# Optimization experiments

Measured on AMD Instinct MI355X. Metric: run time of the kernel, lower is better.

## Reference

```python
import jax, jax.numpy as jnp
import numpy as np

HEADS = 16
D_MODEL = 1024
D_HEAD = D_MODEL // HEADS


def setup_inputs() -> dict:
    key = jax.random.key(0)
    ks = jax.random.split(key, 9)
    s_h = 1.0 / np.sqrt(D_HEAD)
    s_m = 1.0 / np.sqrt(D_MODEL)
    return {
        "x": jax.random.normal(ks[0], (4, 2048, D_MODEL), dtype=jnp.float32),
        "Wq": jax.random.uniform(ks[1], (D_HEAD, D_HEAD), jnp.float32, -s_h, s_h),
        "bq": jax.random.uniform(ks[2], (D_HEAD,), jnp.float32, -s_h, s_h),
        "Wk": jax.random.uniform(ks[3], (D_HEAD, D_HEAD), jnp.float32, -s_h, s_h),
        "bk": jax.random.uniform(ks[4], (D_HEAD,), jnp.float32, -s_h, s_h),
        "Wv": jax.random.uniform(ks[5], (D_HEAD, D_HEAD), jnp.float32, -s_h, s_h),
        "bv": jax.random.uniform(ks[6], (D_HEAD,), jnp.float32, -s_h, s_h),
        "Wp": jax.random.uniform(ks[7], (D_MODEL, D_MODEL), jnp.float32, -s_m, s_m),
        "bp": jax.random.uniform(ks[8], (D_MODEL,), jnp.float32, -s_m, s_m),
    }


def reference(x, Wq, bq, Wk, bk, Wv, bv, Wp, bp):
    B, T, C = x.shape
    xh = x.reshape(B, T, HEADS, D_HEAD)  # [B,T,H,Dh]
    # per-head linear projections (torch Linear: x @ W.T + b)
    q = jnp.einsum('bthd,ed->bhte', xh, Wq) + bq  # [B,H,T,Dh]
    k = jnp.einsum('bthd,ed->bhte', xh, Wk) + bk
    v = jnp.einsum('bthd,ed->bhte', xh, Wv) + bv
    # NOTE: original scales by sqrt(C) = sqrt(d_model), not sqrt(d_head)
    att = jnp.einsum('bhqd,bhkd->bhqk', q, k) / jnp.sqrt(jnp.float32(C))
    att = jax.nn.softmax(att, axis=-1)
    out = jnp.einsum('bhqk,bhkd->bhqd', att, v)  # [B,H,T,Dh]
    out = out.transpose(0, 2, 1, 3).reshape(B, T, C)
    return out @ Wp.T + bp
```

## Files before the change

### kernel.cpp

```cpp
#include <hip/hip_runtime.h>
#include <hip/hip_bf16.h>
#include <cstddef>

#define B_  4
#define T_  2048
#define H_  16
#define DH  64
#define C_  1024
#define BH  64

typedef float  f32x16 __attribute__((ext_vector_type(16)));
typedef __bf16 bf16x8 __attribute__((ext_vector_type(8)));

#define MFMA32(a, b, c) __builtin_amdgcn_mfma_f32_32x32x16_bf16(a, b, c, 0, 0, 0)


__global__ __launch_bounds__(256) void qkv_kernel(
    const float* __restrict__ x,
    const float* __restrict__ Wq, const float* __restrict__ bq,
    const float* __restrict__ Wk, const float* __restrict__ bk,
    const float* __restrict__ Wv, const float* __restrict__ bv,
    __bf16* __restrict__ q, __bf16* __restrict__ k, __bf16* __restrict__ vt)
{
    __shared__ __bf16 Xs[128 * 72];
    __shared__ __bf16 Ws[3][64 * 72];
    __bf16* Vtl = Xs;

    const int tt  = blockIdx.x;
    const int bh  = blockIdx.y;
    const int b   = bh >> 4, h = bh & 15;
    const int t0  = tt * 128;
    const int tid = threadIdx.x;
    const int wave = tid >> 6, lane = tid & 63;
    const int m = lane & 31, hh = lane >> 5;

    #pragma unroll
    for (int i = 0; i < 8; ++i) {
        const int idx = i * 256 + tid;
        const int r = idx >> 4, c = (idx & 15) * 4;
        const float4 x4 = *(const float4*)(x + ((size_t)(b * T_ + t0 + r)) * C_ + h * DH + c);
        const uint lo = ((uint)__builtin_bit_cast(unsigned short, (__bf16)x4.y) << 16)
                      | (uint)__builtin_bit_cast(unsigned short, (__bf16)x4.x);
        const uint hi = ((uint)__builtin_bit_cast(unsigned short, (__bf16)x4.w) << 16)
                      | (uint)__builtin_bit_cast(unsigned short, (__bf16)x4.z);
        *(uint*)&Xs[r * 72 + c]     = lo;
        *(uint*)&Xs[r * 72 + c + 2] = hi;
    }
    #pragma unroll
    for (int i = 0; i < 4; ++i) {
        const int idx = i * 256 + tid;
        const int r = idx >> 4, c = (idx & 15) * 4;
        const float* wsrc[3] = {Wq, Wk, Wv};
        #pragma unroll
        for (int wv_ = 0; wv_ < 3; ++wv_) {
            const float4 w4 = *(const float4*)(wsrc[wv_] + r * 64 + c);
            const uint lo = ((uint)__builtin_bit_cast(unsigned short, (__bf16)w4.y) << 16)
                          | (uint)__builtin_bit_cast(unsigned short, (__bf16)w4.x);
            const uint hi = ((uint)__builtin_bit_cast(unsigned short, (__bf16)w4.w) << 16)
                          | (uint)__builtin_bit_cast(unsigned short, (__bf16)w4.z);
            *(uint*)&Ws[wv_][r * 72 + c]     = lo;
            *(uint*)&Ws[wv_][r * 72 + c + 2] = hi;
        }
    }
    __syncthreads();

    bf16x8 xf[4];
    #pragma unroll
    for (int ks = 0; ks < 4; ++ks)
        xf[ks] = *(const bf16x8*)&Xs[(wave * 32 + m) * 72 + ks * 16 + hh * 8];
    __syncthreads();

    const float s32 = 0.03125f;

    #pragma unroll
    for (int mat = 0; mat < 3; ++mat) {
        f32x16 acc0 = {}, acc1 = {};
        #pragma unroll
        for (int ks = 0; ks < 4; ++ks) {
            const bf16x8 w0 = *(const bf16x8*)&Ws[mat][(m) * 72 + ks * 16 + hh * 8];
            const bf16x8 w1 = *(const bf16x8*)&Ws[mat][(32 + m) * 72 + ks * 16 + hh * 8];
            acc0 = MFMA32(xf[ks], w0, acc0);
            acc1 = MFMA32(xf[ks], w1, acc1);
        }
        const float* bias = (mat == 0) ? bq : (mat == 1) ? bk : bv;
        const float b0 = bias[m], b1 = bias[32 + m];
        #pragma unroll
        for (int r = 0; r < 16; ++r) {
            const int R = (r & 3) + 8 * (r >> 2) + 4 * hh;
            const int tloc = wave * 32 + R;
            const float v0 = acc0[r] + b0, v1 = acc1[r] + b1;
            if (mat == 0) {
                const size_t base = ((size_t)bh * T_ + t0 + tloc) * DH;
                q[base + m]      = (__bf16)(v0 * s32);
                q[base + 32 + m] = (__bf16)(v1 * s32);
            } else if (mat == 1) {
                const size_t base = ((size_t)bh * T_ + t0 + tloc) * DH;
                k[base + m]      = (__bf16)v0;
                k[base + 32 + m] = (__bf16)v1;
            } else {
                Vtl[(m) * 136 + tloc]      = (__bf16)v0;
                Vtl[(32 + m) * 136 + tloc] = (__bf16)v1;
            }
        }
    }
    __syncthreads();
    #pragma unroll
    for (int i = 0; i < 4; ++i) {
        const int idx = i * 256 + tid;
        const int e = idx >> 4, c = (idx & 15) * 8;
        *(uint4*)(vt + ((size_t)(bh * 64 + e)) * T_ + t0 + c) = *(uint4*)&Vtl[e * 136 + c];
    }
}

__global__ __launch_bounds__(256, 3) void attn_kernel(
    const __bf16* __restrict__ q, const __bf16* __restrict__ k,
    const __bf16* __restrict__ vt, __bf16* __restrict__ o)
{
    __shared__ __bf16 Ks[64 * 72];
    __shared__ __bf16 Vts[64 * 72];
    __shared__ __bf16 Ps[128 * 72];

    const int bh  = blockIdx.y;
    const int q0  = blockIdx.x * 128;
    const int tid = threadIdx.x;
    const int wave = tid >> 6, lane = tid & 63;
    const int m = lane & 31, h = lane >> 5;
    const int qrow0 = wave * 32;

    const __bf16* qb = q  + (size_t)bh * T_ * DH;
    const __bf16* kb = k  + (size_t)bh * T_ * DH;
    const __bf16* vb = vt + (size_t)bh * DH * T_;

    #pragma unroll
    for (int i = 0; i < 4; ++i) {
        const int idx = i * 256 + tid;
        const int r = idx >> 3, c = (idx & 7) * 8;
        *(uint4*)&Ps[r * 72 + c] = *(const uint4*)(qb + (size_t)(q0 + r) * DH + c);
    }
    __syncthreads();

    bf16x8 qf[4];
    #pragma unroll
    for (int ks = 0; ks < 4; ++ks)
        qf[ks] = *(const bf16x8*)&Ps[(qrow0 + m) * 72 + ks * 16 + h * 8];

    f32x16 O0 = {}, O1 = {};
    float lsum[16];
    #pragma unroll
    for (int r = 0; r < 16; ++r) lsum[r] = 0.f;

    for (int kt = 0; kt < T_; kt += 64) {
        __syncthreads();
        #pragma unroll
        for (int i = 0; i < 2; ++i) {
            const int idx = i * 256 + tid;
            const int r = idx >> 3, c = (idx & 7) * 8;
            *(uint4*)&Ks[r * 72 + c] = *(const uint4*)(kb + (size_t)(kt + r) * DH + c);
        }
        #pragma unroll
        for (int i = 0; i < 2; ++i) {
            const int idx = i * 256 + tid;
            const int r = idx >> 3, c = (idx & 7) * 8;
            *(uint4*)&Vts[r * 72 + c] = *(const uint4*)(vb + (size_t)r * T_ + kt + c);
        }
        __syncthreads();

        f32x16 S0 = {}, S1 = {};
        #pragma unroll
        for (int ks = 0; ks < 4; ++ks) {
            const bf16x8 k0 = *(const bf16x8*)&Ks[(m) * 72 + ks * 16 + h * 8];
            const bf16x8 k1 = *(const bf16x8*)&Ks[(32 + m) * 72 + ks * 16 + h * 8];
            S0 = MFMA32(qf[ks], k0, S0);
            S1 = MFMA32(qf[ks], k1, S1);
        }

        #pragma unroll
        for (int r = 0; r < 16; ++r) {
            const int R = (r & 3) + 8 * (r >> 2) + 4 * h;
            const float p0 = __expf(S0[r]);
            const float p1 = __expf(S1[r]);
            lsum[r] += p0 + p1;
            Ps[(qrow0 + R) * 72 + m]      = (__bf16)p0;
            Ps[(qrow0 + R) * 72 + 32 + m] = (__bf16)p1;
        }

        #pragma unroll
        for (int ks = 0; ks < 4; ++ks) {
            const bf16x8 pf = *(const bf16x8*)&Ps[(qrow0 + m) * 72 + ks * 16 + h * 8];
            const bf16x8 v0 = *(const bf16x8*)&Vts[(m) * 72 + ks * 16 + h * 8];
            const bf16x8 v1 = *(const bf16x8*)&Vts[(32 + m) * 72 + ks * 16 + h * 8];
            O0 = MFMA32(pf, v0, O0);
            O1 = MFMA32(pf, v1, O1);
        }
    }

    #pragma unroll
    for (int r = 0; r < 16; ++r) {
        float s = lsum[r];
        s += __shfl_xor(s, 1);  s += __shfl_xor(s, 2);  s += __shfl_xor(s, 4);
        s += __shfl_xor(s, 8);  s += __shfl_xor(s, 16);
        lsum[r] = 1.0f / s;
    }
    __bf16* ob = o + (size_t)bh * T_ * DH;
    #pragma unroll
    for (int r = 0; r < 16; ++r) {
        const int R = (r & 3) + 8 * (r >> 2) + 4 * h;
        const size_t row = (size_t)(q0 + qrow0 + R) * DH;
        ob[row + m]      = (__bf16)(O0[r] * lsum[r]);
        ob[row + 32 + m] = (__bf16)(O1[r] * lsum[r]);
    }
}

__global__ __launch_bounds__(256) void proj_kernel(
    const __bf16* __restrict__ a,
    const float* __restrict__ Wp, const float* __restrict__ bp,
    float* __restrict__ out)
{
    __shared__ __bf16 As[128 * 72];
    __shared__ __bf16 Bs[128 * 72];

    const int tb = blockIdx.x, eb = blockIdx.y;
    const int tid = threadIdx.x;
    const int wave = tid >> 6, lane = tid & 63;
    const int m = lane & 31, h = lane >> 5;
    const int tok0 = tb * 128;
    const int b = tok0 >> 11, t0 = tok0 & (T_ - 1);
    const int e0 = eb * 128;

    f32x16 acc[4] = {f32x16{}, f32x16{}, f32x16{}, f32x16{}};

    for (int cb = 0; cb < 16; ++cb) {
        __syncthreads();
        #pragma unroll
        for (int i = 0; i < 4; ++i) {
            const int idx = i * 256 + tid;
            const int r = idx >> 3, c = (idx & 7) * 8;
            *(uint4*)&As[r * 72 + c] =
                *(const uint4*)(a + ((size_t)(b * H_ + cb) * T_ + t0 + r) * DH + c);
        }
        #pragma unroll
        for (int i = 0; i < 8; ++i) {
            const int idx = i * 256 + tid;
            const int r = idx >> 4, c = (idx & 15) * 4;
            const float4 w4 = *(const float4*)(Wp + (size_t)(e0 + r) * C_ + cb * 64 + c);
            const uint lo = ((uint)__builtin_bit_cast(unsigned short, (__bf16)w4.y) << 16)
                          | (uint)__builtin_bit_cast(unsigned short, (__bf16)w4.x);
            const uint hi = ((uint)__builtin_bit_cast(unsigned short, (__bf16)w4.w) << 16)
                          | (uint)__builtin_bit_cast(unsigned short, (__bf16)w4.z);
            *(uint*)&Bs[r * 72 + c]     = lo;
            *(uint*)&Bs[r * 72 + c + 2] = hi;
        }
        __syncthreads();

        #pragma unroll
        for (int ks = 0; ks < 4; ++ks) {
            const bf16x8 af = *(const bf16x8*)&As[(wave * 32 + m) * 72 + ks * 16 + h * 8];
            #pragma unroll
            for (int n = 0; n < 4; ++n) {
                const bf16x8 bf = *(const bf16x8*)&Bs[(n * 32 + m) * 72 + ks * 16 + h * 8];
                acc[n] = MFMA32(af, bf, acc[n]);
            }
        }
    }

    #pragma unroll
    for (int n = 0; n < 4; ++n) {
        const int e = e0 + n * 32 + m;
        const float bias = bp[e];
        #pragma unroll
        for (int r = 0; r < 16; ++r) {
            const int R = (r & 3) + 8 * (r >> 2) + 4 * h;
            out[(size_t)(tok0 + wave * 32 + R) * C_ + e] = acc[n][r] + bias;
        }
    }
}

extern "C" void kernel_launch(void* const* d_in, const int* in_sizes, int n_in,
                              void* d_out, int out_size, void* d_ws, size_t ws_size,
                              hipStream_t stream)
{
    const float* x  = (const float*)d_in[0];
    const float* Wq = (const float*)d_in[1];
    const float* bq = (const float*)d_in[2];
    const float* Wk = (const float*)d_in[3];
    const float* bk = (const float*)d_in[4];
    const float* Wv = (const float*)d_in[5];
    const float* bv = (const float*)d_in[6];
    const float* Wp = (const float*)d_in[7];
    const float* bp = (const float*)d_in[8];

    const size_t N = (size_t)BH * T_ * DH;
    __bf16* qws  = (__bf16*)d_ws;
    __bf16* kws  = qws + N;
    __bf16* vtws = kws + N;
    __bf16* ows  = vtws + N;

    qkv_kernel<<<dim3(16, 64), 256, 0, stream>>>(
        x, Wq, bq, Wk, bk, Wv, bv, qws, kws, vtws);
    attn_kernel<<<dim3(16, 64), 256, 0, stream>>>(qws, kws, vtws, ows);
    proj_kernel<<<dim3(64, 8), 256, 0, stream>>>(ows, Wp, bp, (float*)d_out);
}
```

Baseline: 234.9 us.

## Swizzle LDS tiles, pre-convert Wp to bf16, stage Q/K stores, prefetch tiles to registers

The padded LDS layouts are replaced by an XOR-swizzled 64-wide layout in the attention and projection kernels. Wp is converted to bf16 once inside the QKV kernel, so the projection kernel loads bf16 directly instead of converting fp32 on every tile. Q and K outputs are now staged through LDS so they can be written with coalesced 16-byte stores. Global loads for K/V and A/B tiles are issued into registers before the barrier so they overlap the previous iteration, and the attention occupancy hint is dropped. The cost is extra workspace and extra barriers in the QKV kernel.

```diff
diff --git a/kernel.cpp b/kernel.cpp
--- a/kernel.cpp
+++ b/kernel.cpp
@@ -15,16 +15,25 @@
 #define MFMA32(a, b, c) __builtin_amdgcn_mfma_f32_32x32x16_bf16(a, b, c, 0, 0, 0)
 
 
+__device__ __forceinline__ unsigned pack2(float a, float b) {
+    return ((unsigned)__builtin_bit_cast(unsigned short, (__bf16)b) << 16)
+         | (unsigned)__builtin_bit_cast(unsigned short, (__bf16)a);
+}
+
+__device__ __forceinline__ int sw(int r, int c) {
+    return r * 64 + ((((c >> 3) ^ (r & 7)) << 3) | (c & 7));
+}
+
 __global__ __launch_bounds__(256) void qkv_kernel(
     const float* __restrict__ x,
     const float* __restrict__ Wq, const float* __restrict__ bq,
     const float* __restrict__ Wk, const float* __restrict__ bk,
     const float* __restrict__ Wv, const float* __restrict__ bv,
+    const float* __restrict__ Wp, __bf16* __restrict__ Wp16,
     __bf16* __restrict__ q, __bf16* __restrict__ k, __bf16* __restrict__ vt)
 {
     __shared__ __bf16 Xs[128 * 72];
     __shared__ __bf16 Ws[3][64 * 72];
-    __bf16* Vtl = Xs;
 
     const int tt  = blockIdx.x;
     const int bh  = blockIdx.y;
@@ -34,17 +43,20 @@
     const int wave = tid >> 6, lane = tid & 63;
     const int m = lane & 31, hh = lane >> 5;
 
+    {
+        const int flat = (bh * 16 + tt) * 256 + tid;
+        const float4 w4 = *(const float4*)(Wp + (size_t)flat * 4);
+        uint2 pk; pk.x = pack2(w4.x, w4.y); pk.y = pack2(w4.z, w4.w);
+        *(uint2*)(Wp16 + (size_t)flat * 4) = pk;
+    }
+
     #pragma unroll
     for (int i = 0; i < 8; ++i) {
         const int idx = i * 256 + tid;
         const int r = idx >> 4, c = (idx & 15) * 4;
         const float4 x4 = *(const float4*)(x + ((size_t)(b * T_ + t0 + r)) * C_ + h * DH + c);
-        const uint lo = ((uint)__builtin_bit_cast(unsigned short, (__bf16)x4.y) << 16)
-                      | (uint)__builtin_bit_cast(unsigned short, (__bf16)x4.x);
-        const uint hi = ((uint)__builtin_bit_cast(unsigned short, (__bf16)x4.w) << 16)
-                      | (uint)__builtin_bit_cast(unsigned short, (__bf16)x4.z);
-        *(uint*)&Xs[r * 72 + c]     = lo;
-        *(uint*)&Xs[r * 72 + c + 2] = hi;
+        *(unsigned*)&Xs[r * 72 + c]     = pack2(x4.x, x4.y);
+        *(unsigned*)&Xs[r * 72 + c + 2] = pack2(x4.z, x4.w);
     }
     #pragma unroll
     for (int i = 0; i < 4; ++i) {
@@ -54,12 +66,8 @@
         #pragma unroll
         for (int wv_ = 0; wv_ < 3; ++wv_) {
             const float4 w4 = *(const float4*)(wsrc[wv_] + r * 64 + c);
-            const uint lo = ((uint)__builtin_bit_cast(unsigned short, (__bf16)w4.y) << 16)
-                          | (uint)__builtin_bit_cast(unsigned short, (__bf16)w4.x);
-            const uint hi = ((uint)__builtin_bit_cast(unsigned short, (__bf16)w4.w) << 16)
-                          | (uint)__builtin_bit_cast(unsigned short, (__bf16)w4.z);
-            *(uint*)&Ws[wv_][r * 72 + c]     = lo;
-            *(uint*)&Ws[wv_][r * 72 + c + 2] = hi;
+            *(unsigned*)&Ws[wv_][r * 72 + c]     = pack2(w4.x, w4.y);
+            *(unsigned*)&Ws[wv_][r * 72 + c + 2] = pack2(w4.z, w4.w);
         }
     }
     __syncthreads();
@@ -68,7 +76,6 @@
     #pragma unroll
     for (int ks = 0; ks < 4; ++ks)
         xf[ks] = *(const bf16x8*)&Xs[(wave * 32 + m) * 72 + ks * 16 + hh * 8];
-    __syncthreads();
 
     const float s32 = 0.03125f;
 
@@ -84,41 +91,51 @@
         }
         const float* bias = (mat == 0) ? bq : (mat == 1) ? bk : bv;
         const float b0 = bias[m], b1 = bias[32 + m];
-        #pragma unroll
-        for (int r = 0; r < 16; ++r) {
-            const int R = (r & 3) + 8 * (r >> 2) + 4 * hh;
-            const int tloc = wave * 32 + R;
-            const float v0 = acc0[r] + b0, v1 = acc1[r] + b1;
-            if (mat == 0) {
-                const size_t base = ((size_t)bh * T_ + t0 + tloc) * DH;
-                q[base + m]      = (__bf16)(v0 * s32);
-                q[base + 32 + m] = (__bf16)(v1 * s32);
-            } else if (mat == 1) {
-                const size_t base = ((size_t)bh * T_ + t0 + tloc) * DH;
-                k[base + m]      = (__bf16)v0;
-                k[base + 32 + m] = (__bf16)v1;
-            } else {
-                Vtl[(m) * 136 + tloc]      = (__bf16)v0;
-                Vtl[(32 + m) * 136 + tloc] = (__bf16)v1;
-            }
-        }
-    }
-    __syncthreads();
-    #pragma unroll
-    for (int i = 0; i < 4; ++i) {
-        const int idx = i * 256 + tid;
-        const int e = idx >> 4, c = (idx & 15) * 8;
-        *(uint4*)(vt + ((size_t)(bh * 64 + e)) * T_ + t0 + c) = *(uint4*)&Vtl[e * 136 + c];
-    }
-}
-
-__global__ __launch_bounds__(256, 3) void attn_kernel(
+
+        if (mat < 2) {
+            #pragma unroll
+            for (int r = 0; r < 16; ++r) {
+                const int tloc = wave * 32 + (r & 3) + 8 * (r >> 2) + 4 * hh;
+                const float sc = (mat == 0) ? s32 : 1.0f;
+                Xs[tloc * 72 + m]      = (__bf16)((acc0[r] + b0) * sc);
+                Xs[tloc * 72 + 32 + m] = (__bf16)((acc1[r] + b1) * sc);
+            }
+            __syncthreads();
+            __bf16* dst = (mat == 0) ? q : k;
+            #pragma unroll
+            for (int i = 0; i < 4; ++i) {
+                const int idx = i * 256 + tid;
+                const int r = idx >> 3, c = (idx & 7) * 8;
+                *(uint4*)(dst + ((size_t)bh * T_ + t0 + r) * DH + c) =
+                    *(uint4*)&Xs[r * 72 + c];
+            }
+            __syncthreads();
+        } else {
+            #pragma unroll
+            for (int r = 0; r < 16; ++r) {
+                const int tloc = wave * 32 + (r & 3) + 8 * (r >> 2) + 4 * hh;
+                Xs[(m) * 136 + tloc]      = (__bf16)(acc0[r] + b0);
+                Xs[(32 + m) * 136 + tloc] = (__bf16)(acc1[r] + b1);
+            }
+            __syncthreads();
+            #pragma unroll
+            for (int i = 0; i < 4; ++i) {
+                const int idx = i * 256 + tid;
+                const int e = idx >> 4, c = (idx & 15) * 8;
+                *(uint4*)(vt + ((size_t)(bh * 64 + e)) * T_ + t0 + c) =
+                    *(uint4*)&Xs[e * 136 + c];
+            }
+        }
+    }
+}
+
+__global__ __launch_bounds__(256) void attn_kernel(
     const __bf16* __restrict__ q, const __bf16* __restrict__ k,
     const __bf16* __restrict__ vt, __bf16* __restrict__ o)
 {
-    __shared__ __bf16 Ks[64 * 72];
-    __shared__ __bf16 Vts[64 * 72];
-    __shared__ __bf16 Ps[128 * 72];
+    __shared__ __bf16 PQs[128 * 64];
+    __shared__ __bf16 Ks[64 * 64];
+    __shared__ __bf16 Vts[64 * 64];
 
     const int bh  = blockIdx.y;
     const int q0  = blockIdx.x * 128;
@@ -135,14 +152,14 @@
     for (int i = 0; i < 4; ++i) {
         const int idx = i * 256 + tid;
         const int r = idx >> 3, c = (idx & 7) * 8;
-        *(uint4*)&Ps[r * 72 + c] = *(const uint4*)(qb + (size_t)(q0 + r) * DH + c);
+        *(uint4*)&PQs[sw(r, c)] = *(const uint4*)(qb + (size_t)(q0 + r) * DH + c);
     }
     __syncthreads();
 
     bf16x8 qf[4];
     #pragma unroll
     for (int ks = 0; ks < 4; ++ks)
-        qf[ks] = *(const bf16x8*)&Ps[(qrow0 + m) * 72 + ks * 16 + h * 8];
+        qf[ks] = *(const bf16x8*)&PQs[sw(qrow0 + m, ks * 16 + h * 8)];
 
     f32x16 O0 = {}, O1 = {};
     float lsum[16];
@@ -150,26 +167,29 @@
     for (int r = 0; r < 16; ++r) lsum[r] = 0.f;
 
     for (int kt = 0; kt < T_; kt += 64) {
-        __syncthreads();
+        uint4 kr[2], vr[2];
         #pragma unroll
         for (int i = 0; i < 2; ++i) {
             const int idx = i * 256 + tid;
             const int r = idx >> 3, c = (idx & 7) * 8;
-            *(uint4*)&Ks[r * 72 + c] = *(const uint4*)(kb + (size_t)(kt + r) * DH + c);
-        }
+            kr[i] = *(const uint4*)(kb + (size_t)(kt + r) * DH + c);
+            vr[i] = *(const uint4*)(vb + (size_t)r * T_ + kt + c);
+        }
+        __syncthreads();
         #pragma unroll
         for (int i = 0; i < 2; ++i) {
             const int idx = i * 256 + tid;
             const int r = idx >> 3, c = (idx & 7) * 8;
-            *(uint4*)&Vts[r * 72 + c] = *(const uint4*)(vb + (size_t)r * T_ + kt + c);
+            *(uint4*)&Ks[sw(r, c)]  = kr[i];
+            *(uint4*)&Vts[sw(r, c)] = vr[i];
         }
         __syncthreads();
 
         f32x16 S0 = {}, S1 = {};
         #pragma unroll
         for (int ks = 0; ks < 4; ++ks) {
-            const bf16x8 k0 = *(const bf16x8*)&Ks[(m) * 72 + ks * 16 + h * 8];
-            const bf16x8 k1 = *(const bf16x8*)&Ks[(32 + m) * 72 + ks * 16 + h * 8];
+            const bf16x8 k0 = *(const bf16x8*)&Ks[sw(m,      ks * 16 + h * 8)];
+            const bf16x8 k1 = *(const bf16x8*)&Ks[sw(32 + m, ks * 16 + h * 8)];
             S0 = MFMA32(qf[ks], k0, S0);
             S1 = MFMA32(qf[ks], k1, S1);
         }
@@ -180,15 +200,15 @@
             const float p0 = __expf(S0[r]);
             const float p1 = __expf(S1[r]);
             lsum[r] += p0 + p1;
-            Ps[(qrow0 + R) * 72 + m]      = (__bf16)p0;
-            Ps[(qrow0 + R) * 72 + 32 + m] = (__bf16)p1;
+            PQs[sw(qrow0 + R, m)]      = (__bf16)p0;
+            PQs[sw(qrow0 + R, 32 + m)] = (__bf16)p1;
         }
 
         #pragma unroll
         for (int ks = 0; ks < 4; ++ks) {
-            const bf16x8 pf = *(const bf16x8*)&Ps[(qrow0 + m) * 72 + ks * 16 + h * 8];
-            const bf16x8 v0 = *(const bf16x8*)&Vts[(m) * 72 + ks * 16 + h * 8];
-            const bf16x8 v1 = *(const bf16x8*)&Vts[(32 + m) * 72 + ks * 16 + h * 8];
+            const bf16x8 pf = *(const bf16x8*)&PQs[sw(qrow0 + m, ks * 16 + h * 8)];
+            const bf16x8 v0 = *(const bf16x8*)&Vts[sw(m,      ks * 16 + h * 8)];
+            const bf16x8 v1 = *(const bf16x8*)&Vts[sw(32 + m, ks * 16 + h * 8)];
             O0 = MFMA32(pf, v0, O0);
             O1 = MFMA32(pf, v1, O1);
         }
@@ -213,11 +233,11 @@
 
 __global__ __launch_bounds__(256) void proj_kernel(
     const __bf16* __restrict__ a,
-    const float* __restrict__ Wp, const float* __restrict__ bp,
+    const __bf16* __restrict__ Wp16, const float* __restrict__ bp,
     float* __restrict__ out)
 {
-    __shared__ __bf16 As[128 * 72];
-    __shared__ __bf16 Bs[128 * 72];
+    __shared__ __bf16 As[128 * 64];
+    __shared__ __bf16 Bs[128 * 64];
 
     const int tb = blockIdx.x, eb = blockIdx.y;
     const int tid = threadIdx.x;
@@ -230,34 +250,30 @@
     f32x16 acc[4] = {f32x16{}, f32x16{}, f32x16{}, f32x16{}};
 
     for (int cb = 0; cb < 16; ++cb) {
-        __syncthreads();
+        uint4 ar[4], br[4];
         #pragma unroll
         for (int i = 0; i < 4; ++i) {
             const int idx = i * 256 + tid;
             const int r = idx >> 3, c = (idx & 7) * 8;
-            *(uint4*)&As[r * 72 + c] =
-                *(const uint4*)(a + ((size_t)(b * H_ + cb) * T_ + t0 + r) * DH + c);
-        }
-        #pragma unroll
-        for (int i = 0; i < 8; ++i) {
+            ar[i] = *(const uint4*)(a + ((size_t)(b * H_ + cb) * T_ + t0 + r) * DH + c);
+            br[i] = *(const uint4*)(Wp16 + (size_t)(e0 + r) * C_ + cb * 64 + c);
+        }
+        __syncthreads();
+        #pragma unroll
+        for (int i = 0; i < 4; ++i) {
             const int idx = i * 256 + tid;
-            const int r = idx >> 4, c = (idx & 15) * 4;
-            const float4 w4 = *(const float4*)(Wp + (size_t)(e0 + r) * C_ + cb * 64 + c);
-            const uint lo = ((uint)__builtin_bit_cast(unsigned short, (__bf16)w4.y) << 16)
-                          | (uint)__builtin_bit_cast(unsigned short, (__bf16)w4.x);
-            const uint hi = ((uint)__builtin_bit_cast(unsigned short, (__bf16)w4.w) << 16)
-                          | (uint)__builtin_bit_cast(unsigned short, (__bf16)w4.z);
-            *(uint*)&Bs[r * 72 + c]     = lo;
-            *(uint*)&Bs[r * 72 + c + 2] = hi;
+            const int r = idx >> 3, c = (idx & 7) * 8;
+            *(uint4*)&As[sw(r, c)] = ar[i];
+            *(uint4*)&Bs[sw(r, c)] = br[i];
         }
         __syncthreads();
 
         #pragma unroll
         for (int ks = 0; ks < 4; ++ks) {
-            const bf16x8 af = *(const bf16x8*)&As[(wave * 32 + m) * 72 + ks * 16 + h * 8];
+            const bf16x8 af = *(const bf16x8*)&As[sw(wave * 32 + m, ks * 16 + h * 8)];
             #pragma unroll
             for (int n = 0; n < 4; ++n) {
-                const bf16x8 bf = *(const bf16x8*)&Bs[(n * 32 + m) * 72 + ks * 16 + h * 8];
+                const bf16x8 bf = *(const bf16x8*)&Bs[sw(n * 32 + m, ks * 16 + h * 8)];
                 acc[n] = MFMA32(af, bf, acc[n]);
             }
         }
@@ -294,9 +310,10 @@
     __bf16* kws  = qws + N;
     __bf16* vtws = kws + N;
     __bf16* ows  = vtws + N;
+    __bf16* wp16 = ows + N;
 
     qkv_kernel<<<dim3(16, 64), 256, 0, stream>>>(
-        x, Wq, bq, Wk, bk, Wv, bv, qws, kws, vtws);
+        x, Wq, bq, Wk, bk, Wv, bv, Wp, wp16, qws, kws, vtws);
     attn_kernel<<<dim3(16, 64), 256, 0, stream>>>(qws, kws, vtws, ows);
-    proj_kernel<<<dim3(64, 8), 256, 0, stream>>>(ows, Wp, bp, (float*)d_out);
-}
+    proj_kernel<<<dim3(64, 8), 256, 0, stream>>>(ows, wp16, bp, (float*)d_out);
+}
```

Measured after the change: 348.5 us. 1.48x slower.
